# Optimization experiments

Measured on AMD Instinct MI355X. Metric: run time of the kernel, lower is better.

Reference implementation:

```python
import jax, jax.numpy as jnp
import numpy as np

B, T, J, C = 64, 243, 17, 128   # batch, frames (temporal nodes), joints, channels
K = 4                            # neighbour_num for top-k similarity adjacency
EPS_LN = 1e-5
EPS_BN = 1e-5
S_GCN2ATTN = 0.5                 # fixed (requires_grad=False) scale; dropout is identity in eval


def setup_inputs() -> dict:
    key = jax.random.key(0)
    ks = jax.random.split(key, 4)
    s = np.sqrt(2.0 / C).astype(np.float32)  # GCN weight init scale
    return {
        "x": jax.random.normal(ks[0], (B, T, J, C), jnp.float32),
        "attention_feat": jax.random.normal(ks[1], (B, T, J, C), jnp.float32),
        "ln_w": jnp.ones((C,), jnp.float32),
        "ln_b": jnp.zeros((C,), jnp.float32),
        "Uw": jax.random.normal(ks[2], (C, C), jnp.float32) * s,
        "Ub": jnp.zeros((C,), jnp.float32),
        "Vw": jax.random.normal(ks[3], (C, C), jnp.float32) * s,
        "Vb": jnp.zeros((C,), jnp.float32),
        "bn_w": jnp.ones((T,), jnp.float32),   # BatchNorm1d(num_nodes=T), eval mode
        "bn_b": jnp.zeros((T,), jnp.float32),
        "ls1": jnp.full((C,), 1e-5, jnp.float32),  # layer_scale_1
    }


def reference(x, attention_feat, ln_w, ln_b, Uw, Ub, Vw, Vb, bn_w, bn_b, ls1):
    res = x
    # norm1: LayerNorm over channel dim
    mu = jnp.mean(x, axis=-1, keepdims=True)
    var = jnp.mean(jnp.square(x - mu), axis=-1, keepdims=True)
    xn = (x - mu) * jax.lax.rsqrt(var + EPS_LN) * ln_w + ln_b

    # temporal GCN: (B, T, J, C) -> (B*J, T, C)
    y = jnp.transpose(xn, (0, 2, 1, 3)).reshape(B * J, T, C)

    # dynamic adjacency via top-k similarity
    sim = jnp.einsum('ntc,nsc->nts', y, y)                 # [B*J, T, T]
    thr = jax.lax.top_k(sim, K)[0][..., -1:]               # k-th largest per row
    adj = (sim >= thr).astype(y.dtype)

    # D^{-1/2} A D^{-1/2} (degrees detached in original)
    dinv = jax.lax.stop_gradient(jnp.sum(adj, axis=-1)) ** -0.5  # [B*J, T]
    norm_adj = dinv[:, :, None] * adj * dinv[:, None, :]

    agg = jnp.einsum('nts,nsc->ntc', norm_adj, y @ Vw.T + Vb)
    h = agg + y @ Uw.T + Ub
    # eval-mode BatchNorm1d over T channel (running_mean=0, running_var=1)
    h = h * (bn_w * jax.lax.rsqrt(jnp.asarray(1.0 + EPS_BN, h.dtype)))[None, :, None] + bn_b[None, :, None]
    z = jax.nn.relu(y + h)                                 # dim_in == dim_out residual

    gcn_out = jnp.transpose(z.reshape(B, J, T, C), (0, 2, 1, 3))  # back to [B, T, J, C]

    gx = ls1 * gcn_out                                     # layer_scale_1 (drop_path = identity)
    graph_feat = gx * S_GCN2ATTN                           # gcn2Attn dropout identity in eval
    out = gx + attention_feat + res
    return out, graph_feat
```

## Files before the change

### kernel.cpp

```cpp
#include <hip/hip_runtime.h>

#define B_ 64
#define T_ 243
#define J_ 17
#define C_ 128
#define JC (J_*C_)
#define NTOT (B_*T_*J_*C_)

#define YOFF    0
#define YVOFF   34816
#define NBROFF  69632
#define BNWOFF  70656
#define BNBOFF  71680
#define UBOFF   72704
#define LSOFF   73216
#define SMEM_BYTES 73728
#define YSTR 136

typedef float f32x4 __attribute__((ext_vector_type(4)));
typedef float f32x2 __attribute__((ext_vector_type(2)));

__device__ __forceinline__ unsigned pkf8(float a, float b, float c, float d){
  int p = __builtin_amdgcn_cvt_pk_fp8_f32(a, b, 0, false);
  p = __builtin_amdgcn_cvt_pk_fp8_f32(c, d, p, true);
  return (unsigned)p;
}

template<int CTRL>
__device__ __forceinline__ float dppadd(float v){
  int t = __builtin_amdgcn_update_dpp(0, __float_as_int(v), CTRL, 0xf, 0xf, true);
  return v + __int_as_float(t);
}
__device__ __forceinline__ float swz16(float v){
  return __int_as_float(__builtin_amdgcn_ds_swizzle(__float_as_int(v), 0x401F));
}

#define PINS(x, a0,a1,a2,a3) do { \
  float t_ = fmaxf(a0,(x)), m_ = fminf(a0,(x)); a0 = t_; \
  float t2_ = fmaxf(a1,m_); m_ = fminf(a1,m_); a1 = t2_; \
  float t3_ = fmaxf(a2,m_); m_ = fminf(a2,m_); a2 = t3_; \
  a3 = fmaxf(a3,m_); \
} while(0)
#define MM(p,q) do { float h_=fmaxf(p,q); q=fminf(p,q); p=h_; } while(0)

extern "C" __global__ void __launch_bounds__(512, 4)
graphblock_kernel(const float* __restrict__ x, const float* __restrict__ att,
                  const float* __restrict__ lnw, const float* __restrict__ lnb,
                  const float* __restrict__ Uw, const float* __restrict__ Ubv,
                  const float* __restrict__ Vw, const float* __restrict__ Vbv,
                  const float* __restrict__ bnw, const float* __restrict__ bnb,
                  const float* __restrict__ ls1, float* __restrict__ out)
{
  extern __shared__ char smem[];
  const int tid = threadIdx.x;
  const int w = tid >> 6, l = tid & 63;
  const int lr = l & 15, lg = l >> 4;
  const int n = blockIdx.x, b = n / J_, j = n % J_;
  const long nbase = (long)b*T_*JC + (long)j*C_;
  const int ch0 = w*16 + lg*4;

  if (tid < 256) {
    bool v = tid < T_;
    ((float*)(smem+BNWOFF))[tid] = v ? bnw[tid]*rsqrtf(1.0f+1e-5f) : 0.f;
    ((float*)(smem+BNBOFF))[tid] = v ? bnb[tid] : 0.f;
  } else if (tid < 384) {
    int c = tid - 256;
    ((float*)(smem+UBOFF))[c] = Ubv[c];
    ((float*)(smem+LSOFF))[c] = ls1[c];
  }

  {
    const int lh = l >> 5, lc = l & 31;
    const float4 lw4 = *(const float4*)(lnw + lc*4);
    const float4 lb4 = *(const float4*)(lnb + lc*4);
    #pragma unroll
    for (int g2=0; g2<2; g2++){
      float4 p[8];
      #pragma unroll
      for (int i=0;i<8;i++){
        const int r = (g2*8+i)*16 + w*2 + lh;
        p[i] = make_float4(0.f,0.f,0.f,0.f);
        if (r < T_) p[i] = *(const float4*)(x + nbase + (long)r*JC + lc*4);
      }
      #pragma unroll
      for (int i=0;i<8;i++){
        const int r = (g2*8+i)*16 + w*2 + lh;
        unsigned pk = 0u;
        if (r < T_) {
          float4 v = p[i];
          float s = (v.x+v.y)+(v.z+v.w);
          float q = (v.x*v.x+v.y*v.y)+(v.z*v.z+v.w*v.w);
          s = dppadd<0xB1>(s);  q = dppadd<0xB1>(q);
          s = dppadd<0x4E>(s);  q = dppadd<0x4E>(q);
          s = dppadd<0x124>(s); q = dppadd<0x124>(q);
          s = dppadd<0x128>(s); q = dppadd<0x128>(q);
          s += swz16(s);        q += swz16(q);
          float mu = s*(1.f/128.f);
          float rs = rsqrtf(q*(1.f/128.f)-mu*mu+1e-5f);
          pk = pkf8((v.x-mu)*rs*lw4.x+lb4.x, (v.y-mu)*rs*lw4.y+lb4.y,
                    (v.z-mu)*rs*lw4.z+lb4.z, (v.w-mu)*rs*lw4.w+lb4.w);
        }
        *(unsigned*)(smem + YOFF + r*YSTR + lc*4) = pk;
      }
    }
  }
  __syncthreads();

  #pragma unroll
  for (int half=0; half<2; half++){
    const int tcol = half*128 + w*16 + lr;
    long bfr[4];
    #pragma unroll
    for (int kk=0;kk<4;kk++)
      bfr[kk] = *(const long*)(smem + YOFF + tcol*YSTR + kk*32 + lg*8);
    float v0=-3e38f, v1=-3e38f, v2=-3e38f, v3=-3e38f;
    #pragma unroll 4
    for (int st=0; st<16; st++){
      f32x4 acc = {0.f,0.f,0.f,0.f};
      #pragma unroll
      for (int kk=0;kk<4;kk++){
        long afr = *(const long*)(smem + YOFF + (st*16+lr)*YSTR + kk*32 + lg*8);
        acc = __builtin_amdgcn_mfma_f32_16x16x32_fp8_fp8(afr, bfr[kk], acc, 0,0,0);
      }
      #pragma unroll
      for (int reg=0;reg<4;reg++){
        const int sidx = st*16 + lg*4 + reg;
        unsigned uu = (__float_as_uint(acc[reg]) & 0xffffff00u) | (unsigned)(sidx & 0xff);
        float pv = (sidx < T_) ? __uint_as_float(uu) : -3e38f;
        PINS(pv, v0,v1,v2,v3);
      }
    }
    #pragma unroll
    for (int m=16;m<64;m<<=1){
      float c0=__shfl_xor(v0,m,64), c1=__shfl_xor(v1,m,64),
            c2=__shfl_xor(v2,m,64), c3=__shfl_xor(v3,m,64);
      float d0=fmaxf(v0,c3), d1=fmaxf(v1,c2), d2=fmaxf(v2,c1), d3=fmaxf(v3,c0);
      MM(d0,d1); MM(d2,d3); MM(d0,d2); MM(d1,d3); MM(d1,d2);
      v0=d0; v1=d1; v2=d2; v3=d3;
    }
    if (lg==0){
      unsigned pk = (__float_as_uint(v0) & 0xffu)
                  | ((__float_as_uint(v1) & 0xffu) << 8)
                  | ((__float_as_uint(v2) & 0xffu) << 16)
                  | ((__float_as_uint(v3) & 0xffu) << 24);
      *(unsigned*)(smem + NBROFF + tcol*4) = pk;
    }
  }

  long ufr[4], vfr[4];
  {
    const int crw = w*16 + lr;
    #pragma unroll
    for (int kk=0;kk<4;kk++){
      const float4* pu = (const float4*)(Uw + crw*C_ + kk*32 + lg*8);
      float4 a = pu[0], c = pu[1];
      union { long v; unsigned u[2]; } r;
      r.u[0] = pkf8(a.x,a.y,a.z,a.w); r.u[1] = pkf8(c.x,c.y,c.z,c.w);
      ufr[kk] = r.v;
      const float4* pv = (const float4*)(Vw + crw*C_ + kk*32 + lg*8);
      a = pv[0]; c = pv[1];
      r.u[0] = pkf8(a.x,a.y,a.z,a.w); r.u[1] = pkf8(c.x,c.y,c.z,c.w);
      vfr[kk] = r.v;
    }
  }
  const float4 vb4 = *(const float4*)(Vbv + ch0);

  int    tA[3];  bool okA[3];  long gA[3];
  float4 pxA[3], paA[3];
  #pragma unroll
  for (int i=0;i<3;i++){
    const int t = i*16 + lr;
    tA[i] = t; okA[i] = true;
    gA[i] = nbase + (long)t*JC + ch0;
    pxA[i] = *(const float4*)(x+gA[i]);
    paA[i] = *(const float4*)(att+gA[i]);
  }

  unsigned hu[16];
  #pragma unroll
  for (int tt=0; tt<16; tt++){
    const int t = tt*16 + lr;
    f32x4 accV = {0.f,0.f,0.f,0.f}, accU = {0.f,0.f,0.f,0.f};
    #pragma unroll
    for (int kk=0;kk<4;kk++){
      long yf = *(const long*)(smem + YOFF + t*YSTR + kk*32 + lg*8);
      accU = __builtin_amdgcn_mfma_f32_16x16x32_fp8_fp8(ufr[kk], yf, accU, 0,0,0);
      accV = __builtin_amdgcn_mfma_f32_16x16x32_fp8_fp8(vfr[kk], yf, accV, 0,0,0);
    }
    *(unsigned*)(smem + YVOFF + t*YSTR + ch0) =
        pkf8(0.25f*(accV[0]+vb4.x), 0.25f*(accV[1]+vb4.y),
             0.25f*(accV[2]+vb4.z), 0.25f*(accV[3]+vb4.w));
    hu[tt] = pkf8(accU[0], accU[1], accU[2], accU[3]);
  }
  __syncthreads();

  const float4 ub4 = *(const float4*)((const float*)(smem+UBOFF) + ch0);
  const float4 ls4 = *(const float4*)((const float*)(smem+LSOFF) + ch0);

  #pragma unroll
  for (int tt=0; tt<16; tt++){
    const int slot = tt % 3;
    const int   t  = tA[slot];
    const bool  ok = okA[slot];
    const long  g  = gA[slot];
    const float4 x4 = pxA[slot], a4 = paA[slot];
    if (tt < 13){
      const int tn = (tt+3)*16 + lr;
      tA[slot]  = tn;
      okA[slot] = tn < T_;
      gA[slot]  = nbase + (long)tn*JC + ch0;
      pxA[slot] = make_float4(0,0,0,0); paA[slot] = make_float4(0,0,0,0);
      if (okA[slot]){ pxA[slot] = *(const float4*)(x+gA[slot]); paA[slot] = *(const float4*)(att+gA[slot]); }
    }
    const unsigned nb = *(const unsigned*)(smem + NBROFF + t*4);
    const float bw = ((const float*)(smem+BNWOFF))[t];
    const float bb = ((const float*)(smem+BNBOFF))[t];
    const unsigned yq = *(const unsigned*)(smem + YOFF + t*YSTR + ch0);
    const int s0 = (int)(nb & 0xffu), s1 = (int)((nb>>8)&0xffu),
              s2 = (int)((nb>>16)&0xffu), s3 = (int)((nb>>24)&0xffu);
    float ag0=0,ag1=0,ag2=0,ag3=0;
    {
      unsigned q; f32x2 e, o2;
      q = *(const unsigned*)(smem+YVOFF + s0*YSTR + ch0);
      e = __builtin_amdgcn_cvt_pk_f32_fp8(q,false); o2 = __builtin_amdgcn_cvt_pk_f32_fp8(q,true);
      ag0+=e[0]; ag1+=e[1]; ag2+=o2[0]; ag3+=o2[1];
      q = *(const unsigned*)(smem+YVOFF + s1*YSTR + ch0);
      e = __builtin_amdgcn_cvt_pk_f32_fp8(q,false); o2 = __builtin_amdgcn_cvt_pk_f32_fp8(q,true);
      ag0+=e[0]; ag1+=e[1]; ag2+=o2[0]; ag3+=o2[1];
      q = *(const unsigned*)(smem+YVOFF + s2*YSTR + ch0);
      e = __builtin_amdgcn_cvt_pk_f32_fp8(q,false); o2 = __builtin_amdgcn_cvt_pk_f32_fp8(q,true);
      ag0+=e[0]; ag1+=e[1]; ag2+=o2[0]; ag3+=o2[1];
      q = *(const unsigned*)(smem+YVOFF + s3*YSTR + ch0);
      e = __builtin_amdgcn_cvt_pk_f32_fp8(q,false); o2 = __builtin_amdgcn_cvt_pk_f32_fp8(q,true);
      ag0+=e[0]; ag1+=e[1]; ag2+=o2[0]; ag3+=o2[1];
    }
    float u0,u1,u2,u3, yo0,yo1,yo2,yo3;
    {
      f32x2 e = __builtin_amdgcn_cvt_pk_f32_fp8(hu[tt],false);
      f32x2 o2 = __builtin_amdgcn_cvt_pk_f32_fp8(hu[tt],true);
      u0=e[0]; u1=e[1]; u2=o2[0]; u3=o2[1];
      e = __builtin_amdgcn_cvt_pk_f32_fp8(yq,false);
      o2 = __builtin_amdgcn_cvt_pk_f32_fp8(yq,true);
      yo0=e[0]; yo1=e[1]; yo2=o2[0]; yo3=o2[1];
    }
    f32x4 o, gf;
    {
      float h = (u0 + ag0 + ub4.x)*bw + bb;
      float gx = ls4.x * fmaxf(0.f, yo0 + h);
      o[0] = gx + a4.x + x4.x; gf[0] = gx*0.5f;
    }{
      float h = (u1 + ag1 + ub4.y)*bw + bb;
      float gx = ls4.y * fmaxf(0.f, yo1 + h);
      o[1] = gx + a4.y + x4.y; gf[1] = gx*0.5f;
    }{
      float h = (u2 + ag2 + ub4.z)*bw + bb;
      float gx = ls4.z * fmaxf(0.f, yo2 + h);
      o[2] = gx + a4.z + x4.z; gf[2] = gx*0.5f;
    }{
      float h = (u3 + ag3 + ub4.w)*bw + bb;
      float gx = ls4.w * fmaxf(0.f, yo3 + h);
      o[3] = gx + a4.w + x4.w; gf[3] = gx*0.5f;
    }
    if (ok){
      *(f32x4*)(out+g)      = o;
      *(f32x4*)(out+NTOT+g) = gf;
    }
  }
}

extern "C" void kernel_launch(void* const* d_in, const int* in_sizes, int n_in,
                              void* d_out, int out_size, void* d_ws, size_t ws_size,
                              hipStream_t stream) {
  hipFuncSetAttribute(reinterpret_cast<const void*>(graphblock_kernel),
                      hipFuncAttributeMaxDynamicSharedMemorySize, SMEM_BYTES);
  dim3 grid(B_ * J_);
  dim3 block(512);
  graphblock_kernel<<<grid, block, SMEM_BYTES, stream>>>(
      (const float*)d_in[0],
      (const float*)d_in[1],
      (const float*)d_in[2],
      (const float*)d_in[3],
      (const float*)d_in[4],
      (const float*)d_in[5],
      (const float*)d_in[6],
      (const float*)d_in[7],
      (const float*)d_in[8],
      (const float*)d_in[9],
      (const float*)d_in[10],
      (float*)d_out);
}
```

Measured before the change: 184.9 us.

## Overwrite fp8 Y tile in place with YV to cut LDS and raise occupancy

Drops the separate YV shared-memory buffer and writes the V-projection result back into the Y tile in place. Each thread first caches its own Y element in registers, and a per-row barrier keeps neighbouring reads correct. This roughly halves LDS use, and the launch bound rises from 4 to 6 blocks per CU. The three-deep software prefetch of x/att rows is removed to free registers, at the cost of exposed global-load latency and 16 extra block-wide barriers in the MFMA loop.

Measured after the change: 195.2 us. 5.6% more time.

```diff
diff --git a/kernel.cpp b/kernel.cpp
--- a/kernel.cpp
+++ b/kernel.cpp
@@ -8,13 +8,12 @@
 #define NTOT (B_*T_*J_*C_)
 
 #define YOFF    0
-#define YVOFF   34816
-#define NBROFF  69632
-#define BNWOFF  70656
-#define BNBOFF  71680
-#define UBOFF   72704
-#define LSOFF   73216
-#define SMEM_BYTES 73728
+#define NBROFF  34816
+#define BNWOFF  35840
+#define BNBOFF  36864
+#define UBOFF   37888
+#define LSOFF   38400
+#define SMEM_BYTES 38912
 #define YSTR 136
 
 typedef float f32x4 __attribute__((ext_vector_type(4)));
@@ -43,7 +42,7 @@
 } while(0)
 #define MM(p,q) do { float h_=fmaxf(p,q); q=fminf(p,q); p=h_; } while(0)
 
-extern "C" __global__ void __launch_bounds__(512, 4)
+extern "C" __global__ void __launch_bounds__(512, 6)
 graphblock_kernel(const float* __restrict__ x, const float* __restrict__ att,
                   const float* __restrict__ lnw, const float* __restrict__ lnb,
                   const float* __restrict__ Uw, const float* __restrict__ Ubv,
@@ -165,32 +164,29 @@
   }
   const float4 vb4 = *(const float4*)(Vbv + ch0);
 
-  int    tA[3];  bool okA[3];  long gA[3];
-  float4 pxA[3], paA[3];
-  #pragma unroll
-  for (int i=0;i<3;i++){
-    const int t = i*16 + lr;
-    tA[i] = t; okA[i] = true;
-    gA[i] = nbase + (long)t*JC + ch0;
-    pxA[i] = *(const float4*)(x+gA[i]);
-    paA[i] = *(const float4*)(att+gA[i]);
-  }
-
-  unsigned hu[16];
+  unsigned hu[16], yo[16];
   #pragma unroll
   for (int tt=0; tt<16; tt++){
     const int t = tt*16 + lr;
-    f32x4 accV = {0.f,0.f,0.f,0.f}, accU = {0.f,0.f,0.f,0.f};
-    #pragma unroll
-    for (int kk=0;kk<4;kk++){
-      long yf = *(const long*)(smem + YOFF + t*YSTR + kk*32 + lg*8);
-      accU = __builtin_amdgcn_mfma_f32_16x16x32_fp8_fp8(ufr[kk], yf, accU, 0,0,0);
-      accV = __builtin_amdgcn_mfma_f32_16x16x32_fp8_fp8(vfr[kk], yf, accV, 0,0,0);
-    }
-    *(unsigned*)(smem + YVOFF + t*YSTR + ch0) =
+    long yf0 = *(const long*)(smem + YOFF + t*YSTR +  0 + lg*8);
+    long yf1 = *(const long*)(smem + YOFF + t*YSTR + 32 + lg*8);
+    long yf2 = *(const long*)(smem + YOFF + t*YSTR + 64 + lg*8);
+    long yf3 = *(const long*)(smem + YOFF + t*YSTR + 96 + lg*8);
+    yo[tt] = *(const unsigned*)(smem + YOFF + t*YSTR + ch0);
+    f32x4 accU = {0.f,0.f,0.f,0.f}, accV = {0.f,0.f,0.f,0.f};
+    accU = __builtin_amdgcn_mfma_f32_16x16x32_fp8_fp8(ufr[0], yf0, accU, 0,0,0);
+    accV = __builtin_amdgcn_mfma_f32_16x16x32_fp8_fp8(vfr[0], yf0, accV, 0,0,0);
+    accU = __builtin_amdgcn_mfma_f32_16x16x32_fp8_fp8(ufr[1], yf1, accU, 0,0,0);
+    accV = __builtin_amdgcn_mfma_f32_16x16x32_fp8_fp8(vfr[1], yf1, accV, 0,0,0);
+    accU = __builtin_amdgcn_mfma_f32_16x16x32_fp8_fp8(ufr[2], yf2, accU, 0,0,0);
+    accV = __builtin_amdgcn_mfma_f32_16x16x32_fp8_fp8(vfr[2], yf2, accV, 0,0,0);
+    accU = __builtin_amdgcn_mfma_f32_16x16x32_fp8_fp8(ufr[3], yf3, accU, 0,0,0);
+    accV = __builtin_amdgcn_mfma_f32_16x16x32_fp8_fp8(vfr[3], yf3, accV, 0,0,0);
+    hu[tt] = pkf8(accU[0], accU[1], accU[2], accU[3]);
+    __syncthreads();
+    *(unsigned*)(smem + YOFF + t*YSTR + ch0) =
         pkf8(0.25f*(accV[0]+vb4.x), 0.25f*(accV[1]+vb4.y),
              0.25f*(accV[2]+vb4.z), 0.25f*(accV[3]+vb4.w));
-    hu[tt] = pkf8(accU[0], accU[1], accU[2], accU[3]);
   }
   __syncthreads();
 
@@ -199,38 +195,29 @@
 
   #pragma unroll
   for (int tt=0; tt<16; tt++){
-    const int slot = tt % 3;
-    const int   t  = tA[slot];
-    const bool  ok = okA[slot];
-    const long  g  = gA[slot];
-    const float4 x4 = pxA[slot], a4 = paA[slot];
-    if (tt < 13){
-      const int tn = (tt+3)*16 + lr;
-      tA[slot]  = tn;
-      okA[slot] = tn < T_;
-      gA[slot]  = nbase + (long)tn*JC + ch0;
-      pxA[slot] = make_float4(0,0,0,0); paA[slot] = make_float4(0,0,0,0);
-      if (okA[slot]){ pxA[slot] = *(const float4*)(x+gA[slot]); paA[slot] = *(const float4*)(att+gA[slot]); }
-    }
+    const int t = tt*16 + lr;
+    const bool ok = t < T_;
+    const long g = nbase + (long)t*JC + ch0;
+    float4 x4 = make_float4(0,0,0,0), a4 = make_float4(0,0,0,0);
+    if (ok){ x4 = *(const float4*)(x+g); a4 = *(const float4*)(att+g); }
     const unsigned nb = *(const unsigned*)(smem + NBROFF + t*4);
     const float bw = ((const float*)(smem+BNWOFF))[t];
     const float bb = ((const float*)(smem+BNBOFF))[t];
-    const unsigned yq = *(const unsigned*)(smem + YOFF + t*YSTR + ch0);
     const int s0 = (int)(nb & 0xffu), s1 = (int)((nb>>8)&0xffu),
               s2 = (int)((nb>>16)&0xffu), s3 = (int)((nb>>24)&0xffu);
     float ag0=0,ag1=0,ag2=0,ag3=0;
     {
       unsigned q; f32x2 e, o2;
-      q = *(const unsigned*)(smem+YVOFF + s0*YSTR + ch0);
-      e = __builtin_amdgcn_cvt_pk_f32_fp8(q,false); o2 = __builtin_amdgcn_cvt_pk_f32_fp8(q,true);
-      ag0+=e[0]; ag1+=e[1]; ag2+=o2[0]; ag3+=o2[1];
-      q = *(const unsigned*)(smem+YVOFF + s1*YSTR + ch0);
-      e = __builtin_amdgcn_cvt_pk_f32_fp8(q,false); o2 = __builtin_amdgcn_cvt_pk_f32_fp8(q,true);
-      ag0+=e[0]; ag1+=e[1]; ag2+=o2[0]; ag3+=o2[1];
-      q = *(const unsigned*)(smem+YVOFF + s2*YSTR + ch0);
-      e = __builtin_amdgcn_cvt_pk_f32_fp8(q,false); o2 = __builtin_amdgcn_cvt_pk_f32_fp8(q,true);
-      ag0+=e[0]; ag1+=e[1]; ag2+=o2[0]; ag3+=o2[1];
-      q = *(const unsigned*)(smem+YVOFF + s3*YSTR + ch0);
+      q = *(const unsigned*)(smem + YOFF + s0*YSTR + ch0);
+      e = __builtin_amdgcn_cvt_pk_f32_fp8(q,false); o2 = __builtin_amdgcn_cvt_pk_f32_fp8(q,true);
+      ag0+=e[0]; ag1+=e[1]; ag2+=o2[0]; ag3+=o2[1];
+      q = *(const unsigned*)(smem + YOFF + s1*YSTR + ch0);
+      e = __builtin_amdgcn_cvt_pk_f32_fp8(q,false); o2 = __builtin_amdgcn_cvt_pk_f32_fp8(q,true);
+      ag0+=e[0]; ag1+=e[1]; ag2+=o2[0]; ag3+=o2[1];
+      q = *(const unsigned*)(smem + YOFF + s2*YSTR + ch0);
+      e = __builtin_amdgcn_cvt_pk_f32_fp8(q,false); o2 = __builtin_amdgcn_cvt_pk_f32_fp8(q,true);
+      ag0+=e[0]; ag1+=e[1]; ag2+=o2[0]; ag3+=o2[1];
+      q = *(const unsigned*)(smem + YOFF + s3*YSTR + ch0);
       e = __builtin_amdgcn_cvt_pk_f32_fp8(q,false); o2 = __builtin_amdgcn_cvt_pk_f32_fp8(q,true);
       ag0+=e[0]; ag1+=e[1]; ag2+=o2[0]; ag3+=o2[1];
     }
@@ -239,8 +226,8 @@
       f32x2 e = __builtin_amdgcn_cvt_pk_f32_fp8(hu[tt],false);
       f32x2 o2 = __builtin_amdgcn_cvt_pk_f32_fp8(hu[tt],true);
       u0=e[0]; u1=e[1]; u2=o2[0]; u3=o2[1];
-      e = __builtin_amdgcn_cvt_pk_f32_fp8(yq,false);
-      o2 = __builtin_amdgcn_cvt_pk_f32_fp8(yq,true);
+      e = __builtin_amdgcn_cvt_pk_f32_fp8(yo[tt],false);
+      o2 = __builtin_amdgcn_cvt_pk_f32_fp8(yo[tt],true);
       yo0=e[0]; yo1=e[1]; yo2=o2[0]; yo3=o2[1];
     }
     f32x4 o, gf;
```
